# Kernel optimization log

Measured on AMD Instinct MI355X. Metric: run time of the kernel, lower is better.

Reference implementation:

```python
import jax, jax.numpy as jnp
import numpy as np

B, S, D = 32, 2048, 768   # batch, seq_len, hidden_dim
NL, NF = 512, 64          # num_lines, num_functions


def setup_inputs() -> dict:
    key = jax.random.key(0)
    k = jax.random.split(key, 4)
    hidden_states = jax.random.normal(k[0], (B, S, D), dtype=jnp.float32)
    proj_W = jax.random.normal(k[1], (D, D), dtype=jnp.float32) * 0.02
    proj_b = jnp.zeros((D,), dtype=jnp.float32)
    # start <= end per pair, indices in-range
    line_boundaries = jnp.sort(jax.random.randint(k[2], (B, NL, 2), 0, S), axis=-1)
    function_boundaries = jnp.sort(jax.random.randint(k[3], (B, NF, 2), 0, NL), axis=-1)
    return dict(hidden_states=hidden_states, proj_W=proj_W, proj_b=proj_b,
                line_boundaries=line_boundaries, function_boundaries=function_boundaries)


def segment_mean(x, boundaries):
    """Mean of x[b, start:end] per segment; zeros when start >= end.
    x: [B, S, D]; boundaries: [B, N, 2] -> [B, N, D].
    Uses an exclusive prefix-sum so all segments are reduced in one pass."""
    csum = jnp.concatenate([jnp.zeros_like(x[:, :1]), jnp.cumsum(x, axis=1)], axis=1)  # [B, S+1, D]
    start = boundaries[..., 0]
    end = boundaries[..., 1]
    take = lambda idx: jnp.take_along_axis(csum, idx[..., None], axis=1)  # [B, N, D]
    seg_sum = take(end) - take(start)
    length = (end - start).astype(x.dtype)[..., None]
    return jnp.where(length > 0, seg_sum / jnp.maximum(length, 1.0), jnp.zeros_like(seg_sum))


def reference(hidden_states, proj_W, proj_b, line_boundaries, function_boundaries):
    # CodeEncoder projection of pretrained hidden states (no complexity features)
    token_emb = hidden_states @ proj_W + proj_b                     # [B, S, D]
    # _encode_lines: per-boundary token mean
    line_emb = segment_mean(token_emb, line_boundaries)             # [B, NL, D]
    # _encode_functions: per-boundary line mean
    func_emb = segment_mean(line_emb, function_boundaries)          # [B, NF, D]
    # AdaptiveAvgPool1d(1) over the function axis
    file_emb = jnp.mean(func_emb, axis=1)                           # [B, D]
    return token_emb, line_emb, func_emb, file_emb
```

## Files before the change

kernel.cpp:

```cpp
#include <hip/hip_runtime.h>

#define Bq 32
#define Sq 2048
#define Dq 768
#define NLq 512
#define NFq 64
#define SCHUNKS 16
#define LCHUNKS 8

typedef unsigned short u16;
typedef unsigned int u32;
typedef __attribute__((ext_vector_type(4))) unsigned short us4;
typedef __attribute__((ext_vector_type(4))) unsigned int u32x4;
typedef __attribute__((ext_vector_type(8))) short s16x8;
typedef __attribute__((ext_vector_type(4))) float f32x4;

static __device__ __forceinline__ u16 f2bf(float f) {
  unsigned int u = __builtin_bit_cast(unsigned int, f);
  u += 0x7fffu + ((u >> 16) & 1u);
  return (u16)(u >> 16);
}

static __device__ __forceinline__ void gload16(const void* g, void* l) {
  __builtin_amdgcn_global_load_lds(
      (const __attribute__((address_space(1))) unsigned int*)g,
      (__attribute__((address_space(3))) unsigned int*)l, 16, 0, 0);
}

__global__ __launch_bounds__(256) void wt_kernel(const float* __restrict__ W,
                                                 u16* __restrict__ Wt) {
  int idx = blockIdx.x * 256 + threadIdx.x;
  int n = idx / Dq, k = idx % Dq;
  Wt[idx] = f2bf(W[(size_t)k * Dq + n]);
}

__global__ __launch_bounds__(256, 3) void gemm_kernel(const float* __restrict__ A,
                                                      const u16* __restrict__ Wt,
                                                      const float* __restrict__ bias,
                                                      float* __restrict__ C,
                                                      float* __restrict__ pre,
                                                      float* __restrict__ part16) {
  __shared__ float Asf[2][128 * 32];
  __shared__ u16 Bs[2][128 * 32];
  __shared__ float ps[2][128];
  const int tid = threadIdx.x;
  const int bid = blockIdx.y * gridDim.x + blockIdx.x;
  const int lid = (bid & 7) * 384 + (bid >> 3);
  const int gn0 = (lid % 6) * 128;
  const int gm0 = (lid / 6) * 128;
  const int wave = tid >> 6, lane = tid & 63;
  const int lm = lane & 15, quad = lane >> 4;
  const int wm = (wave & 1) * 64, wn = (wave >> 1) * 64;

  const int arow = tid >> 3;
  const int ah = (tid & 7) ^ (arow & 7);
  const size_t astride = (size_t)Dq * 4;
  const char* ga = (const char*)A + (size_t)(gm0 + arow) * astride + ah * 16;
  const char* gb0 = (const char*)Wt + (size_t)(gn0 + (tid >> 2)) * (Dq * 2) + (tid & 3) * 16;
  const char* gb1 = gb0 + (size_t)64 * (Dq * 2);

  f32x4 acc[4][4] = {};
  const int ax = lm & 7;

  auto stage = [&](int t, int buf) {
    char* lA = (char*)&Asf[buf][0] + wave * 1024;
    char* lB = (char*)&Bs[buf][0] + wave * 1024;
    const char* gat = ga + t * 128;
    gload16(gat, lA);
    gload16(gat + 32 * astride, lA + 4096);
    gload16(gat + 64 * astride, lA + 8192);
    gload16(gat + 96 * astride, lA + 12288);
    gload16(gb0 + t * 64, lB);
    gload16(gb1 + t * 64, lB + 4096);
  };

  stage(0, 0);
  __syncthreads();

  for (int t = 0; t < Dq / 32; ++t) {
    if (t < Dq / 32 - 1) stage(t + 1, (t + 1) & 1);
    const int buf = t & 1;

    s16x8 af[4], bfr[4];
#pragma unroll
    for (int i = 0; i < 4; ++i) {
      const float* rowA = &Asf[buf][(wm + i * 16 + lm) * 32];
      f32x4 alo = *(const f32x4*)(rowA + (((2 * quad) ^ ax) << 2));
      f32x4 ahi = *(const f32x4*)(rowA + (((2 * quad + 1) ^ ax) << 2));
      u32 p0, p1, p2, p3;
      asm("v_cvt_pk_bf16_f32 %0, %1, %2" : "=v"(p0) : "v"(alo.x), "v"(alo.y));
      asm("v_cvt_pk_bf16_f32 %0, %1, %2" : "=v"(p1) : "v"(alo.z), "v"(alo.w));
      asm("v_cvt_pk_bf16_f32 %0, %1, %2" : "=v"(p2) : "v"(ahi.x), "v"(ahi.y));
      asm("v_cvt_pk_bf16_f32 %0, %1, %2" : "=v"(p3) : "v"(ahi.z), "v"(ahi.w));
      u32x4 u;
      u.x = p0; u.y = p1; u.z = p2; u.w = p3;
      af[i] = __builtin_bit_cast(s16x8, u);
    }
#pragma unroll
    for (int i = 0; i < 4; ++i)
      bfr[i] = *(const s16x8*)&Bs[buf][(wn + i * 16 + lm) * 32 + quad * 8];
#pragma unroll
    for (int mi = 0; mi < 4; ++mi)
#pragma unroll
      for (int ni = 0; ni < 4; ++ni)
        acc[mi][ni] = __builtin_amdgcn_mfma_f32_16x16x32_bf16(af[mi], bfr[ni],
                                                              acc[mi][ni], 0, 0, 0);
    __syncthreads();
  }

#pragma unroll
  for (int ni = 0; ni < 4; ++ni) {
    const int gn = gn0 + wn + ni * 16 + lm;
    const float bv = bias[gn];
    float psum = 0.f;
#pragma unroll
    for (int mi = 0; mi < 4; ++mi) {
#pragma unroll
      for (int r = 0; r < 4; ++r) {
        const int gm = gm0 + wm + mi * 16 + quad * 4 + r;
        const float cv = acc[mi][ni][r] + bv;
        C[(size_t)gm * Dq + gn] = cv;
        psum += cv;
      }
    }
    psum += __shfl_xor(psum, 16);
    psum += __shfl_xor(psum, 32);
    if (lane < 16) ps[wave & 1][wn + ni * 16 + lm] = psum;
  }
  __syncthreads();
  if (tid < 128) {
    const int b = gm0 >> 11;
    const int sc = (gm0 >> 7) & 15;
    part16[((size_t)b * SCHUNKS + sc) * Dq + gn0 + tid] = ps[0][tid] + ps[1][tid];
  }

#pragma unroll
  for (int ni = 0; ni < 4; ++ni) {
    const int col = wn + ni * 16 + lm;
    const float bv = bias[gn0 + col];
    float em = wm ? ps[0][col] : 0.f;
#pragma unroll
    for (int mi = 0; mi < 4; ++mi) {
      const float v0 = acc[mi][ni][0] + bv, v1 = acc[mi][ni][1] + bv,
                  v2 = acc[mi][ni][2] + bv, v3 = acc[mi][ni][3] + bv;
      const float qs = v0 + v1 + v2 + v3;
      const float t1 = __shfl_up(qs, 16);
      const float i1 = qs + (quad >= 1 ? t1 : 0.f);
      const float t2 = __shfl_up(i1, 32);
      const float iq = i1 + (quad >= 2 ? t2 : 0.f);
      const float eq = iq - qs;
      const float tot = __shfl(iq, 48 + lm);
      const float base = em + eq;
      em += tot;
      const float P0 = base + v0, P1 = P0 + v1, P2 = P1 + v2, P3 = P2 + v3;
      const size_t rowb = (size_t)(gm0 + wm + mi * 16 + quad * 4) * Dq + gn0 + col;
      pre[rowb] = P0;
      pre[rowb + Dq] = P1;
      pre[rowb + 2 * (size_t)Dq] = P2;
      pre[rowb + 3 * (size_t)Dq] = P3;
    }
  }
}

__global__ __launch_bounds__(256) void scan_kernel(float* __restrict__ p, int C) {
  const int idx = blockIdx.x * 256 + threadIdx.x;
  const int b = idx / Dq, d = idx % Dq;
  float run = 0.f;
  for (int c = 0; c < C; ++c) {
    const size_t o = ((size_t)b * C + c) * Dq + d;
    const float v = p[o];
    p[o] = run;
    run += v;
  }
}

__global__ __launch_bounds__(64) void line_kernel(const float* __restrict__ pre,
                                                  const float* __restrict__ part,
                                                  const int* __restrict__ lb,
                                                  float* __restrict__ lemb,
                                                  float* __restrict__ lpart) {
  __shared__ int sb[128];
  __shared__ float soff[SCHUNKS][64];
  const int lc = blockIdx.x, d64 = blockIdx.y, b = blockIdx.z;
  const int tid = threadIdx.x;
  if (tid < 32)
    ((int4*)sb)[tid] = ((const int4*)(lb + ((size_t)b * NLq + lc * 64) * 2))[tid];
  const int d = d64 * 64 + tid;
#pragma unroll
  for (int sc = 0; sc < SCHUNKS; ++sc)
    soff[sc][tid] = part[((size_t)b * SCHUNKS + sc) * Dq + d];
  __syncthreads();
  const float* pb = pre + (size_t)b * Sq * Dq + d;
  float* le = lemb + ((size_t)b * NLq + lc * 64) * Dq + d;
  float sum = 0.f;
  for (int n0 = 0; n0 < 64; n0 += 8) {
    float vs[8], ve[8];
    int len[8];
#pragma unroll
    for (int i = 0; i < 8; ++i) {
      const int s0 = sb[2 * (n0 + i)], s1 = sb[2 * (n0 + i) + 1];
      len[i] = s1 - s0;
      const int t0 = s0 > 0 ? s0 - 1 : 0;
      const int t1 = s1 > 0 ? s1 - 1 : 0;
      const float a0 = pb[(size_t)t0 * Dq] + soff[t0 >> 7][tid];
      const float a1 = pb[(size_t)t1 * Dq] + soff[t1 >> 7][tid];
      vs[i] = s0 > 0 ? a0 : 0.f;
      ve[i] = a1;
    }
#pragma unroll
    for (int i = 0; i < 8; ++i) {
      const float v = len[i] > 0 ? (ve[i] - vs[i]) / (float)len[i] : 0.f;
      le[(size_t)(n0 + i) * Dq] = v;
      sum += v;
    }
  }
  lpart[((size_t)b * LCHUNKS + lc) * Dq + d] = sum;
}

__global__ __launch_bounds__(256) void lcsum_kernel(const float* __restrict__ lemb,
                                                    const float* __restrict__ lpart,
                                                    float* __restrict__ lcsum) {
  const int lc = blockIdx.x, dc = blockIdx.y, b = blockIdx.z;
  const int d = dc * 256 + threadIdx.x;
  const float* src = lemb + ((size_t)b * NLq + lc * 64) * Dq + d;
  float* dst = lcsum + ((size_t)b * (NLq + 1) + lc * 64 + 1) * Dq + d;
  float run = lpart[((size_t)b * LCHUNKS + lc) * Dq + d];
  if (lc == 0) lcsum[(size_t)b * (NLq + 1) * Dq + d] = 0.f;
  for (int n0 = 0; n0 < 64; n0 += 8) {
    float v[8];
#pragma unroll
    for (int i = 0; i < 8; ++i) v[i] = src[(size_t)(n0 + i) * Dq];
#pragma unroll
    for (int i = 0; i < 8; ++i) {
      run += v[i];
      dst[(size_t)(n0 + i) * Dq] = run;
    }
  }
}

__global__ __launch_bounds__(64) void func_kernel(const float* __restrict__ lcsum,
                                                  const int* __restrict__ fb,
                                                  float* __restrict__ femb,
                                                  float* __restrict__ file) {
  __shared__ int sb[NFq * 2];
  const int tid = threadIdx.x;
  const int d64 = blockIdx.x, b = blockIdx.y;
  const int d = d64 * 64 + tid;
  if (tid < NFq * 2 / 4)
    ((int4*)sb)[tid] = ((const int4*)(fb + (size_t)b * NFq * 2))[tid];
  __syncthreads();
  const float* lc = lcsum + (size_t)b * (NLq + 1) * Dq + d;
  float* fe = femb + (size_t)b * NFq * Dq + d;
  float acc = 0.f;
#pragma unroll 8
  for (int f = 0; f < NFq; ++f) {
    const int l0 = sb[2 * f], l1 = sb[2 * f + 1];
    const float v = l1 > l0 ? (lc[(size_t)l1 * Dq] - lc[(size_t)l0 * Dq]) / (float)(l1 - l0)
                            : 0.f;
    fe[(size_t)f * Dq] = v;
    acc += v;
  }
  file[(size_t)b * Dq + d] = acc * (1.f / (float)NFq);
}

extern "C" void kernel_launch(void* const* d_in, const int* in_sizes, int n_in,
                              void* d_out, int out_size, void* d_ws, size_t ws_size,
                              hipStream_t stream) {
  const float* hs   = (const float*)d_in[0];
  const float* W    = (const float*)d_in[1];
  const float* bias = (const float*)d_in[2];
  const int* lb     = (const int*)d_in[3];
  const int* fb     = (const int*)d_in[4];

  float* out = (float*)d_out;
  float* token = out;
  float* line  = token + (size_t)Bq * Sq * Dq;
  float* func  = line + (size_t)Bq * NLq * Dq;
  float* file  = func + (size_t)Bq * NFq * Dq;

  char* ws = (char*)d_ws;
  float* precsum = (float*)ws;
  float* lcsum   = (float*)(ws + 201498624);
  float* part16  = lcsum;
  u16*   Wt      = (u16*)(ws + 201498624 + 50442240);
  float* lpart   = (float*)Wt;

  wt_kernel<<<(Dq * Dq) / 256, 256, 0, stream>>>(W, Wt);
  gemm_kernel<<<dim3(Dq / 128, (Bq * Sq) / 128), 256, 0, stream>>>(hs, Wt, bias, token,
                                                                   precsum, part16);
  scan_kernel<<<(Bq * Dq) / 256, 256, 0, stream>>>(part16, SCHUNKS);
  line_kernel<<<dim3(LCHUNKS, 12, Bq), 64, 0, stream>>>(precsum, part16, lb, line, lpart);
  scan_kernel<<<(Bq * Dq) / 256, 256, 0, stream>>>(lpart, LCHUNKS);
  lcsum_kernel<<<dim3(LCHUNKS, 3, Bq), 256, 0, stream>>>(line, lpart, lcsum);
  func_kernel<<<dim3(12, Bq), 64, 0, stream>>>(lcsum, fb, func, file);
}
```

Measured before the change: 650.0 us.

## Load GEMM fragments directly from global memory into registers, bypassing LDS

The GEMM main loop no longer stages A and B tiles through shared memory with async global-to-LDS copies and barriers. Each lane now loads its own MFMA fragments straight from global memory into registers, with a two-step register double buffer that prefetches the next K slice while the current one runs. This removes LDS traffic, the swizzle and the per-iteration __syncthreads, and frees LDS for higher occupancy. In exchange, waves that share rows or columns fetch the same data separately, which raises L2/global traffic and uses more registers.

```diff
diff --git a/kernel.cpp b/kernel.cpp
--- a/kernel.cpp
+++ b/kernel.cpp
@@ -10,7 +10,6 @@
 
 typedef unsigned short u16;
 typedef unsigned int u32;
-typedef __attribute__((ext_vector_type(4))) unsigned short us4;
 typedef __attribute__((ext_vector_type(4))) unsigned int u32x4;
 typedef __attribute__((ext_vector_type(8))) short s16x8;
 typedef __attribute__((ext_vector_type(4))) float f32x4;
@@ -19,12 +18,6 @@
   unsigned int u = __builtin_bit_cast(unsigned int, f);
   u += 0x7fffu + ((u >> 16) & 1u);
   return (u16)(u >> 16);
-}
-
-static __device__ __forceinline__ void gload16(const void* g, void* l) {
-  __builtin_amdgcn_global_load_lds(
-      (const __attribute__((address_space(1))) unsigned int*)g,
-      (__attribute__((address_space(3))) unsigned int*)l, 16, 0, 0);
 }
 
 __global__ __launch_bounds__(256) void wt_kernel(const float* __restrict__ W,
@@ -40,8 +33,6 @@
                                                       float* __restrict__ C,
                                                       float* __restrict__ pre,
                                                       float* __restrict__ part16) {
-  __shared__ float Asf[2][128 * 32];
-  __shared__ u16 Bs[2][128 * 32];
   __shared__ float ps[2][128];
   const int tid = threadIdx.x;
   const int bid = blockIdx.y * gridDim.x + blockIdx.x;
@@ -52,60 +43,72 @@
   const int lm = lane & 15, quad = lane >> 4;
   const int wm = (wave & 1) * 64, wn = (wave >> 1) * 64;
 
-  const int arow = tid >> 3;
-  const int ah = (tid & 7) ^ (arow & 7);
-  const size_t astride = (size_t)Dq * 4;
-  const char* ga = (const char*)A + (size_t)(gm0 + arow) * astride + ah * 16;
-  const char* gb0 = (const char*)Wt + (size_t)(gn0 + (tid >> 2)) * (Dq * 2) + (tid & 3) * 16;
-  const char* gb1 = gb0 + (size_t)64 * (Dq * 2);
+  const char* __restrict__ Ab = (const char*)A;
+  const char* __restrict__ Bb = (const char*)Wt;
+  u32 aoff[4], boff[4];
+#pragma unroll
+  for (int i = 0; i < 4; ++i) {
+    aoff[i] = (u32)((gm0 + wm + i * 16 + lm) * (Dq * 4) + quad * 32);
+    boff[i] = (u32)((gn0 + wn + i * 16 + lm) * (Dq * 2) + quad * 16);
+  }
 
   f32x4 acc[4][4] = {};
-  const int ax = lm & 7;
-
-  auto stage = [&](int t, int buf) {
-    char* lA = (char*)&Asf[buf][0] + wave * 1024;
-    char* lB = (char*)&Bs[buf][0] + wave * 1024;
-    const char* gat = ga + t * 128;
-    gload16(gat, lA);
-    gload16(gat + 32 * astride, lA + 4096);
-    gload16(gat + 64 * astride, lA + 8192);
-    gload16(gat + 96 * astride, lA + 12288);
-    gload16(gb0 + t * 64, lB);
-    gload16(gb1 + t * 64, lB + 4096);
-  };
-
-  stage(0, 0);
-  __syncthreads();
-
-  for (int t = 0; t < Dq / 32; ++t) {
-    if (t < Dq / 32 - 1) stage(t + 1, (t + 1) & 1);
-    const int buf = t & 1;
-
-    s16x8 af[4], bfr[4];
+  f32x4 aF[4][2];
+  u32x4 bC[4], bN[4];
+
+  auto loadA = [&](int off) {
 #pragma unroll
     for (int i = 0; i < 4; ++i) {
-      const float* rowA = &Asf[buf][(wm + i * 16 + lm) * 32];
-      f32x4 alo = *(const f32x4*)(rowA + (((2 * quad) ^ ax) << 2));
-      f32x4 ahi = *(const f32x4*)(rowA + (((2 * quad + 1) ^ ax) << 2));
+      aF[i][0] = *(const f32x4*)(Ab + (size_t)aoff[i] + off);
+      aF[i][1] = *(const f32x4*)(Ab + (size_t)aoff[i] + off + 16);
+    }
+  };
+  auto loadB = [&](u32x4 (&dst)[4], int off) {
+#pragma unroll
+    for (int i = 0; i < 4; ++i)
+      dst[i] = *(const u32x4*)(Bb + (size_t)boff[i] + off);
+  };
+  auto cvtA = [&](s16x8 (&af)[4]) {
+#pragma unroll
+    for (int i = 0; i < 4; ++i) {
       u32 p0, p1, p2, p3;
-      asm("v_cvt_pk_bf16_f32 %0, %1, %2" : "=v"(p0) : "v"(alo.x), "v"(alo.y));
-      asm("v_cvt_pk_bf16_f32 %0, %1, %2" : "=v"(p1) : "v"(alo.z), "v"(alo.w));
-      asm("v_cvt_pk_bf16_f32 %0, %1, %2" : "=v"(p2) : "v"(ahi.x), "v"(ahi.y));
-      asm("v_cvt_pk_bf16_f32 %0, %1, %2" : "=v"(p3) : "v"(ahi.z), "v"(ahi.w));
+      asm("v_cvt_pk_bf16_f32 %0, %1, %2" : "=v"(p0) : "v"(aF[i][0].x), "v"(aF[i][0].y));
+      asm("v_cvt_pk_bf16_f32 %0, %1, %2" : "=v"(p1) : "v"(aF[i][0].z), "v"(aF[i][0].w));
+      asm("v_cvt_pk_bf16_f32 %0, %1, %2" : "=v"(p2) : "v"(aF[i][1].x), "v"(aF[i][1].y));
+      asm("v_cvt_pk_bf16_f32 %0, %1, %2" : "=v"(p3) : "v"(aF[i][1].z), "v"(aF[i][1].w));
       u32x4 u;
       u.x = p0; u.y = p1; u.z = p2; u.w = p3;
       af[i] = __builtin_bit_cast(s16x8, u);
     }
-#pragma unroll
-    for (int i = 0; i < 4; ++i)
-      bfr[i] = *(const s16x8*)&Bs[buf][(wn + i * 16 + lm) * 32 + quad * 8];
+  };
+  auto domfma = [&](s16x8 (&af)[4], u32x4 (&bb)[4]) {
 #pragma unroll
     for (int mi = 0; mi < 4; ++mi)
 #pragma unroll
       for (int ni = 0; ni < 4; ++ni)
-        acc[mi][ni] = __builtin_amdgcn_mfma_f32_16x16x32_bf16(af[mi], bfr[ni],
-                                                              acc[mi][ni], 0, 0, 0);
-    __syncthreads();
+        acc[mi][ni] = __builtin_amdgcn_mfma_f32_16x16x32_bf16(
+            af[mi], __builtin_bit_cast(s16x8, bb[ni]), acc[mi][ni], 0, 0, 0);
+  };
+
+  loadA(0);
+  loadB(bC, 0);
+
+  for (int t = 0; t < Dq / 32; t += 2) {
+    s16x8 af0[4];
+    cvtA(af0);
+    loadA(128);
+    loadB(bN, 64);
+    domfma(af0, bC);
+
+    s16x8 af1[4];
+    cvtA(af1);
+    if (t + 2 < Dq / 32) {
+      loadA(256);
+      loadB(bC, 128);
+    }
+#pragma unroll
+    for (int i = 0; i < 4; ++i) { aoff[i] += 256; boff[i] += 128; }
+    domfma(af1, bN);
   }
 
 #pragma unroll
```

Result: slower. 849.6 us (+30.7%).
